# Kernel optimization log

Measured on AMD Instinct MI355X. Metric: run time of the kernel, lower is better.

Reference implementation:

```python
import jax, jax.numpy as jnp
import numpy as np

N = 100_000      # nodes
E = 3_200_000    # directed edges (avg degree 32)
F_IN = 5         # node_features
H = 64           # hidden_dim


def setup_inputs() -> dict:
    key = jax.random.key(0)
    ks = jax.random.split(key, 11)
    x = jax.random.uniform(ks[0], (N, F_IN), dtype=jnp.float32)
    edge_index = jax.random.randint(ks[1], (2, E), 0, N, dtype=jnp.int32)
    def lin(k, fi, fo):
        kw, kb = jax.random.split(k)
        s = 1.0 / np.sqrt(fi)
        return (jax.random.uniform(kw, (fi, fo), jnp.float32, -s, s),
                jax.random.uniform(kb, (fo,), jnp.float32, -s, s))
    conv1_w, conv1_b = lin(ks[2], F_IN, H)
    conv2_w, conv2_b = lin(ks[3], H, H)
    lin1_w, lin1_b = lin(ks[4], H + 6, 32)
    lin2_w, lin2_b = lin(ks[5], 32, 2)
    return {"x": x, "edge_index": edge_index,
            "conv1_w": conv1_w, "conv1_b": conv1_b,
            "conv2_w": conv2_w, "conv2_b": conv2_b,
            "lin1_w": lin1_w, "lin1_b": lin1_b,
            "lin2_w": lin2_w, "lin2_b": lin2_b}


def _gcn_conv(x, src, dst, norm, W, b):
    # PyG GCNConv: out[dst] += norm_e * (x @ W)[src], then + bias
    h = x @ W                                   # [N, out]
    msg = h[src] * norm[:, None]                # [E+N, out] (gather, memory-bound)
    out = jax.ops.segment_sum(msg, dst, num_segments=N)
    return out + b


def _global_features(x):
    n_comp = jnp.sum(x[:, 2])
    n_and = jnp.sum(x[:, 3])
    n_or = jnp.sum(x[:, 4])
    comp_mask = (x[:, 2] == 1.0).astype(x.dtype)
    cnt = jnp.sum(comp_mask)
    safe = jnp.maximum(cnt, 1.0)
    avg_lambda = jnp.where(cnt > 0, jnp.sum(x[:, 0] * comp_mask) / safe, 0.0)
    avg_mu = jnp.where(cnt > 0, jnp.sum(x[:, 1] * comp_mask) / safe, 0.0)
    depth = n_and + n_or
    gf = jnp.stack([n_comp, n_and, n_or, depth, avg_lambda, avg_mu])[None, :]
    # original uses .item() -> constants, so no grad flows through these
    return jax.lax.stop_gradient(gf)


def reference(x, edge_index, conv1_w, conv1_b, conv2_w, conv2_b,
              lin1_w, lin1_b, lin2_w, lin2_b):
    loop = jnp.arange(N, dtype=edge_index.dtype)
    src = jnp.concatenate([edge_index[0], loop])   # add self-loops
    dst = jnp.concatenate([edge_index[1], loop])
    deg = jax.ops.segment_sum(jnp.ones_like(src, dtype=x.dtype), dst, num_segments=N)
    dinv = jnp.where(deg > 0, 1.0 / jnp.sqrt(deg), 0.0)
    norm = dinv[src] * dinv[dst]                   # [E+N]

    h = jax.nn.relu(_gcn_conv(x, src, dst, norm, conv1_w, conv1_b))
    h = jax.nn.relu(_gcn_conv(h, src, dst, norm, conv2_w, conv2_b))

    # global_mean_pool with batch == zeros -> mean over all nodes, one graph
    emb = jnp.mean(h, axis=0, keepdims=True)       # [1, H]
    emb = jnp.concatenate([emb, _global_features(x)], axis=1)  # [1, H+6]

    hid = jax.nn.relu(emb @ lin1_w + lin1_b)
    raw = hid @ lin2_w + lin2_b                    # [1, 2]
    return 2.0 + jax.nn.sigmoid(raw) * 3.0
```

## Files before the change

### kernel.cpp

```cpp
#include <hip/hip_runtime.h>
#include <hip/hip_bf16.h>
#include <math.h>


#define BUCKET 256
#define MAXB   512
#define NCHV   2048
#define Q      8
#define RCOPY  32

__global__ void k_hist(const int* __restrict__ dst, int E, int chunk,
                       int* __restrict__ gcounts, int NBK) {
    __shared__ int lcnt[MAXB];
    for (int i = threadIdx.x; i < NBK; i += blockDim.x) lcnt[i] = 0;
    __syncthreads();
    int e0 = blockIdx.x * chunk;
    int e1 = min(e0 + chunk, E);
    for (int e = e0 + threadIdx.x; e < e1; e += blockDim.x)
        atomicAdd(&lcnt[dst[e] >> 8], 1);
    __syncthreads();
    for (int b = threadIdx.x; b < NBK; b += blockDim.x)
        gcounts[blockIdx.x * NBK + b] = lcnt[b];
}

__global__ void k_colsum(const int* __restrict__ gcounts, int* __restrict__ btot,
                         int NBK, int NCH) {
    __shared__ int lds[256];
    int b = blockIdx.x, t = threadIdx.x;
    int s = 0;
    for (int c = t; c < NCH; c += 256) s += gcounts[c * NBK + b];
    lds[t] = s;
    __syncthreads();
    for (int off = 128; off; off >>= 1) {
        if (t < off) lds[t] += lds[t + off];
        __syncthreads();
    }
    if (t == 0) btot[b] = lds[0];
}

__global__ void k_scanA(const int* __restrict__ btot, int* __restrict__ bucket_base,
                        float* __restrict__ red, int* __restrict__ ssrc,
                        int E, int n, int NBK) {
    __shared__ int lds[MAXB];
    int t = threadIdx.x;
    for (int i = t; i < RCOPY * 64; i += MAXB) red[i] = 0.f;
    if (t == 0) ssrc[E] = n;
    int v = (t < NBK) ? btot[t] : 0;
    lds[t] = v;
    __syncthreads();
    for (int off = 1; off < MAXB; off <<= 1) {
        int add = (t >= off) ? lds[t - off] : 0;
        __syncthreads();
        lds[t] += add;
        __syncthreads();
    }
    if (t < NBK) bucket_base[t] = lds[t] - v;
    if (t == NBK - 1) bucket_base[NBK] = lds[t];
}

__global__ void k_scanB(int* __restrict__ gcounts, const int* __restrict__ bucket_base,
                        int NBK, int NCH) {
    __shared__ int lds[512];
    int b = blockIdx.x, t = threadIdx.x;
    int carry = bucket_base[b];
    for (int base = 0; base < NCH; base += 512) {
        int c = base + t;
        int v = (c < NCH) ? gcounts[c * NBK + b] : 0;
        lds[t] = v;
        __syncthreads();
        for (int off = 1; off < 512; off <<= 1) {
            int add = (t >= off) ? lds[t - off] : 0;
            __syncthreads();
            lds[t] += add;
            __syncthreads();
        }
        if (c < NCH) gcounts[c * NBK + b] = carry + lds[t] - v;
        int tot = lds[511];
        __syncthreads();
        carry += tot;
    }
}

__global__ void k_bucketize(const int* __restrict__ src, const int* __restrict__ dst,
                            int E, int chunk, const int* __restrict__ gcounts,
                            int* __restrict__ records, int NBK) {
    __shared__ int lcur[MAXB];
    for (int b = threadIdx.x; b < NBK; b += blockDim.x)
        lcur[b] = gcounts[blockIdx.x * NBK + b];
    __syncthreads();
    int e0 = blockIdx.x * chunk;
    int e1 = min(e0 + chunk, E);
    for (int e = e0 + threadIdx.x; e < e1; e += blockDim.x) {
        int d = dst[e];
        int b = d >> 8;
        int rec = ((d & 255) << 17) | src[e];
        int slot = atomicAdd(&lcur[b], 1);
        records[slot] = rec;
    }
}

__global__ void k_csrA(const int* __restrict__ records, const int* __restrict__ bucket_base,
                       int* __restrict__ qhist) {
    __shared__ int cnt[BUCKET];
    int t = threadIdx.x, b = blockIdx.x, q = blockIdx.y;
    if (t < BUCKET) cnt[t] = 0;
    __syncthreads();
    int j0 = bucket_base[b], j1 = bucket_base[b + 1];
    int qlen = (j1 - j0 + Q - 1) / Q;
    int qs = j0 + q * qlen;
    int qe = min(qs + qlen, j1);
    for (int j = qs + t; j < qe; j += blockDim.x)
        atomicAdd(&cnt[records[j] >> 17], 1);
    __syncthreads();
    if (t < BUCKET) qhist[(b * Q + q) * BUCKET + t] = cnt[t];
}

__global__ void k_csrB(const int* __restrict__ qhist, const int* __restrict__ bucket_base,
                       const float* __restrict__ x,
                       int* __restrict__ qbase, int* __restrict__ pos,
                       int* __restrict__ rowend, float* __restrict__ dinv,
                       float* __restrict__ xs, float* __restrict__ gfpart, int n) {
    __shared__ int lds[BUCKET];
    __shared__ float gf6[8];
    int t = threadIdx.x, b = blockIdx.x;
    if (t < 8) gf6[t] = 0.f;
    int h[Q];
    int c = 0;
#pragma unroll
    for (int q = 0; q < Q; ++q) {
        h[q] = qhist[(b * Q + q) * BUCKET + t];
        c += h[q];
    }
    lds[t] = c;
    __syncthreads();
    for (int off = 1; off < BUCKET; off <<= 1) {
        int add = (t >= off) ? lds[t - off] : 0;
        __syncthreads();
        lds[t] += add;
        __syncthreads();
    }
    int j0 = bucket_base[b];
    int p = j0 + lds[t] - c;
    int run = p;
#pragma unroll
    for (int q = 0; q < Q; ++q) {
        qbase[(b * Q + q) * BUCKET + t] = run;
        run += h[q];
    }
    int node = b * BUCKET + t;
    float s2 = 0.f, s3 = 0.f, s4 = 0.f, sm0 = 0.f, sm1 = 0.f, sc = 0.f;
    if (node < n) {
        pos[node] = p;
        rowend[node] = p + c;
        float d = rsqrtf((float)(c + 1));
        dinv[node] = d;
        float x0 = x[node * 5 + 0], x1 = x[node * 5 + 1], x2 = x[node * 5 + 2];
        float x3 = x[node * 5 + 3], x4 = x[node * 5 + 4];
        float4 o;
        o.x = x0 * d; o.y = x1 * d; o.z = x2 * d; o.w = x3 * d;
        ((float4*)xs)[node * 2] = o;
        xs[node * 8 + 4] = x4 * d;
        s2 = x2; s3 = x3; s4 = x4;
        if (x2 == 1.0f) { sm0 = x0; sm1 = x1; sc = 1.f; }
    }
#pragma unroll
    for (int off = 32; off; off >>= 1) {
        s2 += __shfl_down(s2, off);
        s3 += __shfl_down(s3, off);
        s4 += __shfl_down(s4, off);
        sm0 += __shfl_down(sm0, off);
        sm1 += __shfl_down(sm1, off);
        sc += __shfl_down(sc, off);
    }
    if ((t & 63) == 0) {
        atomicAdd(&gf6[0], s2);
        atomicAdd(&gf6[1], s3);
        atomicAdd(&gf6[2], s4);
        atomicAdd(&gf6[3], sm0);
        atomicAdd(&gf6[4], sm1);
        atomicAdd(&gf6[5], sc);
    }
    __syncthreads();
    if (t < 6) gfpart[b * 8 + t] = gf6[t];
}

__global__ void k_csrC(const int* __restrict__ records, const int* __restrict__ bucket_base,
                       const int* __restrict__ qbase, int* __restrict__ ssrc) {
    __shared__ int cursor[BUCKET];
    int t = threadIdx.x, b = blockIdx.x, q = blockIdx.y;
    if (t < BUCKET) cursor[t] = qbase[(b * Q + q) * BUCKET + t];
    __syncthreads();
    int j0 = bucket_base[b], j1 = bucket_base[b + 1];
    int qlen = (j1 - j0 + Q - 1) / Q;
    int qs = j0 + q * qlen;
    int qe = min(qs + qlen, j1);
    for (int j = qs + t; j < qe; j += blockDim.x) {
        int rec = records[j];
        int slot = atomicAdd(&cursor[rec >> 17], 1);
        ssrc[slot] = rec & 131071;
    }
}

__global__ void k_agg5(const int* __restrict__ pos, const int* __restrict__ rowend,
                       const int* __restrict__ ssrc, const float* __restrict__ dinv,
                       const float* __restrict__ xs, float* __restrict__ agg5, int n) {
    int i = blockIdx.x * blockDim.x + threadIdx.x;
    if (i >= n) return;
    const float4* xs4 = (const float4*)xs;
    float4 a = xs4[i * 2];
    float a4 = xs[i * 8 + 4];
    int beg = pos[i], end = rowend[i];
    int j = beg;
    for (; j + 1 < end; j += 2) {
        int s0 = ssrc[j], s1 = ssrc[j + 1];
        float4 v0 = xs4[s0 * 2]; float w0 = xs[s0 * 8 + 4];
        float4 v1 = xs4[s1 * 2]; float w1 = xs[s1 * 8 + 4];
        a.x += v0.x + v1.x; a.y += v0.y + v1.y;
        a.z += v0.z + v1.z; a.w += v0.w + v1.w;
        a4 += w0 + w1;
    }
    for (; j < end; ++j) {
        int s = ssrc[j];
        float4 v = xs4[s * 2];
        a.x += v.x; a.y += v.y; a.z += v.z; a.w += v.w;
        a4 += xs[s * 8 + 4];
    }
    float dd = dinv[i];
    float4 o; o.x = a.x * dd; o.y = a.y * dd; o.z = a.z * dd; o.w = a.w * dd;
    ((float4*)agg5)[i * 2] = o;
    agg5[i * 8 + 4] = a4 * dd;
}

__global__ void k_h1(const float* __restrict__ agg5, const float* __restrict__ W1,
                     const float* __restrict__ b1, const float* __restrict__ dinv,
                     unsigned char* __restrict__ h1f8, int n) {
    int t = blockIdx.x * blockDim.x + threadIdx.x;
    int i = t >> 6, f = t & 63;
    if (i > n) return;
    if (i == n) {
        h1f8[(size_t)i * 64 + f] = 0;
        return;
    }
    float a0 = agg5[i * 8 + 0], a1 = agg5[i * 8 + 1], a2 = agg5[i * 8 + 2];
    float a3 = agg5[i * 8 + 3], a4 = agg5[i * 8 + 4];
    float v = a0 * W1[f] + a1 * W1[64 + f] + a2 * W1[128 + f]
            + a3 * W1[192 + f] + a4 * W1[256 + f] + b1[f];
    float hv = dinv[i] * fmaxf(v, 0.f);
    int packed = __builtin_amdgcn_cvt_pk_fp8_f32(hv, hv, 0, false);
    h1f8[(size_t)i * 64 + f] = (unsigned char)(packed & 0xFF);
}

__global__ __launch_bounds__(256)
void k_l2fuse(const int* __restrict__ pos, const int* __restrict__ rowend,
              const int* __restrict__ ssrc, const float* __restrict__ dinv,
              const unsigned char* __restrict__ h1f8, const float* __restrict__ W2,
              const float* __restrict__ b2, float* __restrict__ red, int n, int E) {
    __shared__ float red64[64];
    int t = threadIdx.x, f = t & 63;
    if (t < 64) red64[t] = 0.f;
    __syncthreads();
    int w = blockIdx.x * (blockDim.x >> 6) + (t >> 6);
    int nw = gridDim.x * (blockDim.x >> 6);
    float bf = b2[f];
    float psum = 0.f;
    int nt = (n + 3) >> 2;
    for (int task = w; task < nt; task += nw) {
        int i0 = task * 4, i1 = i0 + 1, i2 = i0 + 2, i3 = i0 + 3;
        bool v1 = i1 < n, v2 = i2 < n, v3 = i3 < n;
        int p0 = pos[i0],            e0 = rowend[i0];
        int p1 = v1 ? pos[i1] : 0,   e1 = v1 ? rowend[i1] : 0;
        int p2 = v2 ? pos[i2] : 0,   e2 = v2 ? rowend[i2] : 0;
        int p3 = v3 ? pos[i3] : 0,   e3 = v3 ? rowend[i3] : 0;
        float a0 = __builtin_amdgcn_cvt_f32_fp8(h1f8[(size_t)i0 * 64 + f], 0);
        float a1 = v1 ? __builtin_amdgcn_cvt_f32_fp8(h1f8[(size_t)i1 * 64 + f], 0) : 0.f;
        float a2 = v2 ? __builtin_amdgcn_cvt_f32_fp8(h1f8[(size_t)i2 * 64 + f], 0) : 0.f;
        float a3 = v3 ? __builtin_amdgcn_cvt_f32_fp8(h1f8[(size_t)i3 * 64 + f], 0) : 0.f;
        int len = max(max(e0 - p0, e1 - p1), max(e2 - p2, e3 - p3));
#pragma unroll 2
        for (int m = 0; m < len; ++m) {
            int j0 = p0 + m, j1 = p1 + m, j2 = p2 + m, j3 = p3 + m;
            int s0 = ssrc[j0 < e0 ? j0 : E];
            int s1 = ssrc[j1 < e1 ? j1 : E];
            int s2 = ssrc[j2 < e2 ? j2 : E];
            int s3 = ssrc[j3 < e3 ? j3 : E];
            a0 += __builtin_amdgcn_cvt_f32_fp8(h1f8[(size_t)s0 * 64 + f], 0);
            a1 += __builtin_amdgcn_cvt_f32_fp8(h1f8[(size_t)s1 * 64 + f], 0);
            a2 += __builtin_amdgcn_cvt_f32_fp8(h1f8[(size_t)s2 * 64 + f], 0);
            a3 += __builtin_amdgcn_cvt_f32_fp8(h1f8[(size_t)s3 * 64 + f], 0);
        }
        float q0 = 0.f, q1 = 0.f, q2 = 0.f, q3 = 0.f;
#pragma unroll 8
        for (int k = 0; k < 64; ++k) {
            float w2v = W2[k * 64 + f];
            q0 += __shfl(a0, k) * w2v;
            q1 += __shfl(a1, k) * w2v;
            q2 += __shfl(a2, k) * w2v;
            q3 += __shfl(a3, k) * w2v;
        }
        psum += fmaxf(q0 * dinv[i0] + bf, 0.f);
        if (v1) psum += fmaxf(q1 * dinv[i1] + bf, 0.f);
        if (v2) psum += fmaxf(q2 * dinv[i2] + bf, 0.f);
        if (v3) psum += fmaxf(q3 * dinv[i3] + bf, 0.f);
    }
    atomicAdd(&red64[f], psum);
    __syncthreads();
    if (t < 64) atomicAdd(&red[(blockIdx.x & (RCOPY - 1)) * 64 + t], red64[t]);
}

__global__ void k_head(const float* __restrict__ red, const float* __restrict__ gfpart,
                       const float* __restrict__ l1w, const float* __restrict__ l1b,
                       const float* __restrict__ l2w, const float* __restrict__ l2b,
                       float* __restrict__ out, int n, int NBK) {
    __shared__ float emb[70];
    __shared__ float hid[32];
    int t = threadIdx.x;
    if (t < 64) {
        float s = 0.f;
#pragma unroll
        for (int c = 0; c < RCOPY; ++c) s += red[c * 64 + t];
        emb[t] = s / (float)n;
    }
    float g0 = 0.f, g1 = 0.f, g2 = 0.f, g3 = 0.f, g4 = 0.f, g5 = 0.f;
    for (int b = t; b < NBK; b += 64) {
        g0 += gfpart[b * 8 + 0]; g1 += gfpart[b * 8 + 1];
        g2 += gfpart[b * 8 + 2]; g3 += gfpart[b * 8 + 3];
        g4 += gfpart[b * 8 + 4]; g5 += gfpart[b * 8 + 5];
    }
#pragma unroll
    for (int off = 32; off; off >>= 1) {
        g0 += __shfl_down(g0, off); g1 += __shfl_down(g1, off);
        g2 += __shfl_down(g2, off); g3 += __shfl_down(g3, off);
        g4 += __shfl_down(g4, off); g5 += __shfl_down(g5, off);
    }
    if (t == 0) {
        float cnt = g5;
        float safe = fmaxf(cnt, 1.f);
        emb[64] = g0;
        emb[65] = g1;
        emb[66] = g2;
        emb[67] = g1 + g2;
        emb[68] = cnt > 0.f ? g3 / safe : 0.f;
        emb[69] = cnt > 0.f ? g4 / safe : 0.f;
    }
    __syncthreads();
    if (t < 32) {
        float acc = l1b[t];
#pragma unroll
        for (int k = 0; k < 70; ++k) acc += emb[k] * l1w[k * 32 + t];
        hid[t] = fmaxf(acc, 0.f);
    }
    __syncthreads();
    if (t < 2) {
        float acc = l2b[t];
#pragma unroll
        for (int j = 0; j < 32; ++j) acc += hid[j] * l2w[j * 2 + t];
        out[t] = 2.0f + 3.0f / (1.0f + expf(-acc));
    }
}

extern "C" void kernel_launch(void* const* d_in, const int* in_sizes, int n_in,
                              void* d_out, int out_size, void* d_ws, size_t ws_size,
                              hipStream_t stream) {
    const float* x   = (const float*)d_in[0];
    const int*   ei  = (const int*)d_in[1];
    const float* w1  = (const float*)d_in[2];
    const float* b1  = (const float*)d_in[3];
    const float* w2  = (const float*)d_in[4];
    const float* b2  = (const float*)d_in[5];
    const float* l1w = (const float*)d_in[6];
    const float* l1b = (const float*)d_in[7];
    const float* l2w = (const float*)d_in[8];
    const float* l2b = (const float*)d_in[9];

    const int n = in_sizes[0] / 5;
    const int E = in_sizes[1] / 2;
    const int* src = ei;
    const int* dst = ei + E;

    const int NBK = (n + BUCKET - 1) / BUCKET;
    const int NCH = NCHV;
    const int chunk = (E + NCH - 1) / NCH;

    size_t nf = (size_t)(n + 1) * 64;
    unsigned char* h1f8 = (unsigned char*)d_ws;
    float* xs          = (float*)(h1f8 + ((nf + 255) & ~(size_t)255));
    float* agg5        = xs + (size_t)n * 8;
    float* dinv        = agg5 + (size_t)n * 8;
    float* red         = dinv + n;
    float* gfpart      = red + RCOPY * 64;
    int*   pos         = (int*)(gfpart + (MAXB * 8));
    int*   rowend      = pos + n;
    int*   btot        = rowend + n;
    int*   bucket_base = btot + MAXB;
    int*   qhist       = bucket_base + (MAXB + 8);
    int*   qbase       = qhist + NBK * Q * BUCKET;
    int*   gcounts     = qbase + NBK * Q * BUCKET;
    int*   records     = gcounts + NCH * NBK;
    int*   ssrc        = records + E;

    k_hist<<<NCH, 512, 0, stream>>>(dst, E, chunk, gcounts, NBK);
    k_colsum<<<NBK, 256, 0, stream>>>(gcounts, btot, NBK, NCH);
    k_scanA<<<1, MAXB, 0, stream>>>(btot, bucket_base, red, ssrc, E, n, NBK);
    k_scanB<<<NBK, 512, 0, stream>>>(gcounts, bucket_base, NBK, NCH);
    k_bucketize<<<NCH, 512, 0, stream>>>(src, dst, E, chunk, gcounts, records, NBK);

    dim3 qgrid(NBK, Q);
    k_csrA<<<qgrid, 512, 0, stream>>>(records, bucket_base, qhist);
    k_csrB<<<NBK, BUCKET, 0, stream>>>(qhist, bucket_base, x, qbase, pos, rowend,
                                       dinv, xs, gfpart, n);
    k_csrC<<<qgrid, 512, 0, stream>>>(records, bucket_base, qbase, ssrc);

    k_agg5<<<(n + 255) / 256, 256, 0, stream>>>(pos, rowend, ssrc, dinv, xs, agg5, n);
    k_h1<<<(int)((nf + 255) / 256), 256, 0, stream>>>(agg5, w1, b1, dinv, h1f8, n);

    k_l2fuse<<<4096, 256, 0, stream>>>(pos, rowend, ssrc, dinv, h1f8, w2, b2, red, n, E);

    k_head<<<1, 64, 0, stream>>>(red, gfpart, l1w, l1b, l2w, l2b, (float*)d_out, n, NBK);
}
```

Baseline: 257.7 us.

## Gather fp8 rows as 32-bit words with 16 lanes per node in layer-2 fuse

Restructures the layer-2 aggregation so each 64-lane wave handles four nodes with 16 lanes per node. Each lane loads four packed fp8 features as one 32-bit word, in place of one byte per lane per feature. The per-node edge loop now runs on that node's own degree, which removes the padded lockstep loop over four nodes and the sentinel ssrc[E] entry. The 64x64 matvec reads W2 as float4 and uses shuffles within each 16-lane group. Lanes of a wave still diverge when node degrees differ, and each lane now keeps four accumulators.

```diff
diff --git a/kernel.cpp b/kernel.cpp
--- a/kernel.cpp
+++ b/kernel.cpp
@@ -39,12 +39,10 @@
 }
 
 __global__ void k_scanA(const int* __restrict__ btot, int* __restrict__ bucket_base,
-                        float* __restrict__ red, int* __restrict__ ssrc,
-                        int E, int n, int NBK) {
+                        float* __restrict__ red, int NBK) {
     __shared__ int lds[MAXB];
     int t = threadIdx.x;
     for (int i = t; i < RCOPY * 64; i += MAXB) red[i] = 0.f;
-    if (t == 0) ssrc[E] = n;
     int v = (t < NBK) ? btot[t] : 0;
     lds[t] = v;
     __syncthreads();
@@ -254,55 +252,75 @@
 void k_l2fuse(const int* __restrict__ pos, const int* __restrict__ rowend,
               const int* __restrict__ ssrc, const float* __restrict__ dinv,
               const unsigned char* __restrict__ h1f8, const float* __restrict__ W2,
-              const float* __restrict__ b2, float* __restrict__ red, int n, int E) {
+              const float* __restrict__ b2, float* __restrict__ red, int n) {
     __shared__ float red64[64];
-    int t = threadIdx.x, f = t & 63;
+    int t = threadIdx.x;
+    int lane = t & 63;
+    int g = lane >> 4;
+    int fl = lane & 15;
+    int f0 = fl * 4;
     if (t < 64) red64[t] = 0.f;
     __syncthreads();
+    const unsigned int* h1u = (const unsigned int*)h1f8;
+    float4 bv = *(const float4*)&b2[f0];
+    int gbase = lane & 48;
     int w = blockIdx.x * (blockDim.x >> 6) + (t >> 6);
     int nw = gridDim.x * (blockDim.x >> 6);
-    float bf = b2[f];
-    float psum = 0.f;
+    float p0 = 0.f, p1 = 0.f, p2 = 0.f, p3 = 0.f;
     int nt = (n + 3) >> 2;
     for (int task = w; task < nt; task += nw) {
-        int i0 = task * 4, i1 = i0 + 1, i2 = i0 + 2, i3 = i0 + 3;
-        bool v1 = i1 < n, v2 = i2 < n, v3 = i3 < n;
-        int p0 = pos[i0],            e0 = rowend[i0];
-        int p1 = v1 ? pos[i1] : 0,   e1 = v1 ? rowend[i1] : 0;
-        int p2 = v2 ? pos[i2] : 0,   e2 = v2 ? rowend[i2] : 0;
-        int p3 = v3 ? pos[i3] : 0,   e3 = v3 ? rowend[i3] : 0;
-        float a0 = __builtin_amdgcn_cvt_f32_fp8(h1f8[(size_t)i0 * 64 + f], 0);
-        float a1 = v1 ? __builtin_amdgcn_cvt_f32_fp8(h1f8[(size_t)i1 * 64 + f], 0) : 0.f;
-        float a2 = v2 ? __builtin_amdgcn_cvt_f32_fp8(h1f8[(size_t)i2 * 64 + f], 0) : 0.f;
-        float a3 = v3 ? __builtin_amdgcn_cvt_f32_fp8(h1f8[(size_t)i3 * 64 + f], 0) : 0.f;
-        int len = max(max(e0 - p0, e1 - p1), max(e2 - p2, e3 - p3));
-#pragma unroll 2
-        for (int m = 0; m < len; ++m) {
-            int j0 = p0 + m, j1 = p1 + m, j2 = p2 + m, j3 = p3 + m;
-            int s0 = ssrc[j0 < e0 ? j0 : E];
-            int s1 = ssrc[j1 < e1 ? j1 : E];
-            int s2 = ssrc[j2 < e2 ? j2 : E];
-            int s3 = ssrc[j3 < e3 ? j3 : E];
-            a0 += __builtin_amdgcn_cvt_f32_fp8(h1f8[(size_t)s0 * 64 + f], 0);
-            a1 += __builtin_amdgcn_cvt_f32_fp8(h1f8[(size_t)s1 * 64 + f], 0);
-            a2 += __builtin_amdgcn_cvt_f32_fp8(h1f8[(size_t)s2 * 64 + f], 0);
-            a3 += __builtin_amdgcn_cvt_f32_fp8(h1f8[(size_t)s3 * 64 + f], 0);
+        int i = task * 4 + g;
+        bool vi = i < n;
+        int ci = vi ? i : n;
+        int p = vi ? pos[i] : 0;
+        int e = vi ? rowend[i] : 0;
+        unsigned int u = h1u[(size_t)ci * 16 + fl];
+        float a0 = __builtin_amdgcn_cvt_f32_fp8(u, 0);
+        float a1 = __builtin_amdgcn_cvt_f32_fp8(u, 1);
+        float a2 = __builtin_amdgcn_cvt_f32_fp8(u, 2);
+        float a3 = __builtin_amdgcn_cvt_f32_fp8(u, 3);
+        int j = p;
+        for (; j + 1 < e; j += 2) {
+            int s0 = ssrc[j], s1 = ssrc[j + 1];
+            unsigned int u0 = h1u[(size_t)s0 * 16 + fl];
+            unsigned int u1 = h1u[(size_t)s1 * 16 + fl];
+            a0 += __builtin_amdgcn_cvt_f32_fp8(u0, 0) + __builtin_amdgcn_cvt_f32_fp8(u1, 0);
+            a1 += __builtin_amdgcn_cvt_f32_fp8(u0, 1) + __builtin_amdgcn_cvt_f32_fp8(u1, 1);
+            a2 += __builtin_amdgcn_cvt_f32_fp8(u0, 2) + __builtin_amdgcn_cvt_f32_fp8(u1, 2);
+            a3 += __builtin_amdgcn_cvt_f32_fp8(u0, 3) + __builtin_amdgcn_cvt_f32_fp8(u1, 3);
+        }
+        if (j < e) {
+            int s = ssrc[j];
+            unsigned int uu = h1u[(size_t)s * 16 + fl];
+            a0 += __builtin_amdgcn_cvt_f32_fp8(uu, 0);
+            a1 += __builtin_amdgcn_cvt_f32_fp8(uu, 1);
+            a2 += __builtin_amdgcn_cvt_f32_fp8(uu, 2);
+            a3 += __builtin_amdgcn_cvt_f32_fp8(uu, 3);
         }
         float q0 = 0.f, q1 = 0.f, q2 = 0.f, q3 = 0.f;
-#pragma unroll 8
+#pragma unroll
         for (int k = 0; k < 64; ++k) {
-            float w2v = W2[k * 64 + f];
-            q0 += __shfl(a0, k) * w2v;
-            q1 += __shfl(a1, k) * w2v;
-            q2 += __shfl(a2, k) * w2v;
-            q3 += __shfl(a3, k) * w2v;
+            float ak;
+            if ((k & 3) == 0) ak = a0;
+            else if ((k & 3) == 1) ak = a1;
+            else if ((k & 3) == 2) ak = a2;
+            else ak = a3;
+            ak = __shfl(ak, gbase + (k >> 2));
+            float4 wv = *(const float4*)&W2[k * 64 + f0];
+            q0 += ak * wv.x; q1 += ak * wv.y; q2 += ak * wv.z; q3 += ak * wv.w;
         }
-        psum += fmaxf(q0 * dinv[i0] + bf, 0.f);
-        if (v1) psum += fmaxf(q1 * dinv[i1] + bf, 0.f);
-        if (v2) psum += fmaxf(q2 * dinv[i2] + bf, 0.f);
-        if (v3) psum += fmaxf(q3 * dinv[i3] + bf, 0.f);
-    }
-    atomicAdd(&red64[f], psum);
+        if (vi) {
+            float dd = dinv[i];
+            p0 += fmaxf(q0 * dd + bv.x, 0.f);
+            p1 += fmaxf(q1 * dd + bv.y, 0.f);
+            p2 += fmaxf(q2 * dd + bv.z, 0.f);
+            p3 += fmaxf(q3 * dd + bv.w, 0.f);
+        }
+    }
+    atomicAdd(&red64[f0 + 0], p0);
+    atomicAdd(&red64[f0 + 1], p1);
+    atomicAdd(&red64[f0 + 2], p2);
+    atomicAdd(&red64[f0 + 3], p3);
     __syncthreads();
     if (t < 64) atomicAdd(&red[(blockIdx.x & (RCOPY - 1)) * 64 + t], red64[t]);
 }
@@ -400,7 +418,7 @@
 
     k_hist<<<NCH, 512, 0, stream>>>(dst, E, chunk, gcounts, NBK);
     k_colsum<<<NBK, 256, 0, stream>>>(gcounts, btot, NBK, NCH);
-    k_scanA<<<1, MAXB, 0, stream>>>(btot, bucket_base, red, ssrc, E, n, NBK);
+    k_scanA<<<1, MAXB, 0, stream>>>(btot, bucket_base, red, NBK);
     k_scanB<<<NBK, 512, 0, stream>>>(gcounts, bucket_base, NBK, NCH);
     k_bucketize<<<NCH, 512, 0, stream>>>(src, dst, E, chunk, gcounts, records, NBK);
 
@@ -413,7 +431,7 @@
     k_agg5<<<(n + 255) / 256, 256, 0, stream>>>(pos, rowend, ssrc, dinv, xs, agg5, n);
     k_h1<<<(int)((nf + 255) / 256), 256, 0, stream>>>(agg5, w1, b1, dinv, h1f8, n);
 
-    k_l2fuse<<<4096, 256, 0, stream>>>(pos, rowend, ssrc, dinv, h1f8, w2, b2, red, n, E);
+    k_l2fuse<<<4096, 256, 0, stream>>>(pos, rowend, ssrc, dinv, h1f8, w2, b2, red, n);
 
     k_head<<<1, 64, 0, stream>>>(red, gfpart, l1w, l1b, l2w, l2b, (float*)d_out, n, NBK);
 }
```

After: 619.1 us. 140% more time.
